# Performance work log

Hardware: AMD Instinct MI355X
Metric: run time of the kernel (lower is better)

Reference implementation:

```python
import jax, jax.numpy as jnp
import numpy as np

B, N, D, H, MLP = 8, 1024, 1024, 16, 4096
DEPTH = D // H
EPS = 1e-6
INV_SQRT_DEPTH = 1.0 / np.sqrt(DEPTH).astype(np.float32)


def _linear_params(key, fan_in, fan_out):
    w = jax.random.normal(key, (fan_in, fan_out), dtype=jnp.float32) * 0.02
    b = jnp.zeros((fan_out,), dtype=jnp.float32)
    return w, b


def setup_inputs() -> dict:
    key = jax.random.key(0)
    ks = jax.random.split(key, 20)
    inp = {}
    inp['inputs'] = jax.random.normal(ks[0], (B, N, D), dtype=jnp.float32)
    inp['z'] = jax.random.normal(ks[1], (B, D), dtype=jnp.float32)
    # norm1 conditioning MLPs
    inp['n1_hw'], inp['n1_hb'] = _linear_params(ks[2], D, D)
    inp['n1_gw'], inp['n1_gb'] = _linear_params(ks[3], D, D)
    inp['n1_bw'], inp['n1_bb'] = _linear_params(ks[4], D, D)
    # attention
    inp['wq_w'], inp['wq_b'] = _linear_params(ks[5], D, D)
    inp['wk_w'], inp['wk_b'] = _linear_params(ks[6], D, D)
    inp['wv_w'], inp['wv_b'] = _linear_params(ks[7], D, D)
    inp['qa_w'], inp['qa_b'] = _linear_params(ks[8], D, H)
    inp['out_w'], inp['out_b'] = _linear_params(ks[9], D, D)
    # norm2 conditioning MLPs
    inp['n2_hw'], inp['n2_hb'] = _linear_params(ks[10], D, D)
    inp['n2_gw'], inp['n2_gb'] = _linear_params(ks[11], D, D)
    inp['n2_bw'], inp['n2_bb'] = _linear_params(ks[12], D, D)
    # MLP
    inp['mlp_w1'], inp['mlp_b1'] = _linear_params(ks[13], D, MLP)
    inp['mlp_w2'], inp['mlp_b2'] = _linear_params(ks[14], MLP, D)
    return inp


def _sm_norm(x, z, hw, hb, gw, gb, bw, bb):
    # LayerNorm over last dim, no affine
    mean = jnp.mean(x, axis=-1, keepdims=True)
    var = jnp.mean(jnp.square(x - mean), axis=-1, keepdims=True)
    xn = (x - mean) / jnp.sqrt(var + EPS)
    h = jax.nn.relu(z @ hw + hb)                 # [B, D]
    scale = (h @ gw + gb)[:, :, None]            # [B, D, 1]
    shift = (h @ bw + bb)[:, :, None]            # [B, D, 1]
    # broadcasts since N == D (as in the torch module)
    return xn * scale + shift


def _additive_attn(x, wq_w, wq_b, wk_w, wk_b, wv_w, wv_b, qa_w, qa_b, out_w, out_b):
    q = x @ wq_w + wq_b                          # [B, N, D]
    k = x @ wk_w + wk_b
    v = x @ wv_w + wv_b
    attn = jnp.transpose(q @ qa_w + qa_b, (0, 2, 1)) * INV_SQRT_DEPTH  # [B, H, N]
    attn = jax.nn.softmax(attn, axis=-1)
    qh = q.reshape(B, N, H, DEPTH).transpose(0, 2, 1, 3)  # [B, H, N, d]
    kh = k.reshape(B, N, H, DEPTH).transpose(0, 2, 1, 3)
    vh = v.reshape(B, N, H, DEPTH).transpose(0, 2, 1, 3)
    global_q = jnp.einsum('bhn,bhnd->bhd', attn, qh)[:, :, None, :]  # [B, H, 1, d]
    r = global_q * kh * vh                       # [B, H, N, d]
    r = r.transpose(0, 2, 1, 3).reshape(B, N, D)
    return r @ out_w + out_b, attn


def reference(inputs, z,
              n1_hw, n1_hb, n1_gw, n1_gb, n1_bw, n1_bb,
              wq_w, wq_b, wk_w, wk_b, wv_w, wv_b, qa_w, qa_b, out_w, out_b,
              n2_hw, n2_hb, n2_gw, n2_gb, n2_bw, n2_bb,
              mlp_w1, mlp_b1, mlp_w2, mlp_b2):
    x_norm1 = _sm_norm(inputs, z, n1_hw, n1_hb, n1_gw, n1_gb, n1_bw, n1_bb)
    attn_out, attn_maps = _additive_attn(x_norm1, wq_w, wq_b, wk_w, wk_b,
                                         wv_w, wv_b, qa_w, qa_b, out_w, out_b)
    attn_out = inputs + attn_out                 # dropout rate 0 -> identity
    x_norm2 = _sm_norm(attn_out, z, n2_hw, n2_hb, n2_gw, n2_gb, n2_bw, n2_bb)
    h = jax.nn.gelu(x_norm2 @ mlp_w1 + mlp_b1, approximate=False)
    mlp_out = h @ mlp_w2 + mlp_b2
    output = attn_out + mlp_out
    return output, attn_maps
```

## Files before the change

kernel.cpp:

```cpp
#include <hip/hip_runtime.h>
#include <math.h>


typedef __attribute__((ext_vector_type(8))) short short8;
typedef __attribute__((ext_vector_type(4))) float f32x4;

#define DEVI __device__ __forceinline__

DEVI unsigned short f2bf(float f) {
  union { float f; unsigned int u; } c; c.f = f;
  unsigned int r = c.u + 0x7fffu + ((c.u >> 16) & 1u);
  return (unsigned short)(r >> 16);
}
DEVI float bf2f(unsigned short u) {
  union { unsigned int u; float f; } c; c.u = ((unsigned int)u) << 16;
  return c.f;
}

DEVI void async16(const void* g, void* l) {
  __builtin_amdgcn_global_load_lds((const __attribute__((address_space(1))) void*)g,
                                   (__attribute__((address_space(3))) void*)l, 16, 0, 0);
}

__global__ void transpose_bf16_k(const float* __restrict__ in,
                                 unsigned short* __restrict__ out, int R, int C) {
  __shared__ float tile[32][33];
  const int c0 = blockIdx.x * 32, r0 = blockIdx.y * 32;
  const int tx = threadIdx.x, ty = threadIdx.y;
#pragma unroll
  for (int j = 0; j < 4; j++) {
    int r = r0 + ty + j * 8, c = c0 + tx;
    if (r < R && c < C) tile[ty + j * 8][tx] = in[(size_t)r * C + c];
  }
  __syncthreads();
#pragma unroll
  for (int j = 0; j < 4; j++) {
    int c = c0 + ty + j * 8, r = r0 + tx;
    if (c < C && r < R) out[(size_t)c * R + r] = f2bf(tile[tx][ty + j * 8]);
  }
}

__global__ void pad_bias_k(const float* __restrict__ qa_b, float* __restrict__ pad) {
  int t = threadIdx.x;
  pad[t] = (t < 16) ? qa_b[t] : 0.f;
}

__global__ void zero_k(float4* __restrict__ p) {
  p[blockIdx.x * 256 + threadIdx.x] = float4{0.f, 0.f, 0.f, 0.f};
}

template <int NMAT>
__global__ __launch_bounds__(256) void skinny_k(const float* __restrict__ X,
                                                const float* __restrict__ W0,
                                                const float* __restrict__ W1,
                                                float* __restrict__ acc0,
                                                float* __restrict__ acc1) {
  const int tid = threadIdx.x;
  const int jt = blockIdx.x, kc = blockIdx.y;
  const int jl = tid & 63, kg = tid >> 6;
  const int jcol = jt * 64 + jl;
  __shared__ float xs[8][64];
  for (int i = tid; i < 512; i += 256) {
    const int b = i >> 6, kk = i & 63;
    xs[b][kk] = X[b * 1024 + kc * 64 + kk];
  }
  __syncthreads();
  float a0[8], a1[8];
#pragma unroll
  for (int b = 0; b < 8; b++) { a0[b] = 0.f; a1[b] = 0.f; }
#pragma unroll
  for (int kk = 0; kk < 16; kk++) {
    const int k = kg * 16 + kk;
    const float w0 = W0[(size_t)(kc * 64 + k) * 1024 + jcol];
#pragma unroll
    for (int b = 0; b < 8; b++) a0[b] += xs[b][k] * w0;
    if (NMAT == 2) {
      const float w1 = W1[(size_t)(kc * 64 + k) * 1024 + jcol];
#pragma unroll
      for (int b = 0; b < 8; b++) a1[b] += xs[b][k] * w1;
    }
  }
  __shared__ float red[256][9];
#pragma unroll
  for (int b = 0; b < 8; b++) red[tid][b] = a0[b];
  __syncthreads();
  if (tid < 64) {
#pragma unroll
    for (int b = 0; b < 8; b++) {
      const float s = red[tid][b] + red[tid + 64][b] + red[tid + 128][b] + red[tid + 192][b];
      atomicAdd(&acc0[b * 1024 + jcol], s);
    }
  }
  if (NMAT == 2) {
    __syncthreads();
#pragma unroll
    for (int b = 0; b < 8; b++) red[tid][b] = a1[b];
    __syncthreads();
    if (tid < 64) {
#pragma unroll
      for (int b = 0; b < 8; b++) {
        const float s = red[tid][b] + red[tid + 64][b] + red[tid + 128][b] + red[tid + 192][b];
        atomicAdd(&acc1[b * 1024 + jcol], s);
      }
    }
  }
}

__global__ void h_epi_k(const float* __restrict__ acc, const float* __restrict__ hb,
                        float* __restrict__ h) {
  const int i = blockIdx.x * 256 + threadIdx.x;
  h[i] = fmaxf(acc[i] + hb[i & 1023], 0.f);
}

__global__ __launch_bounds__(256) void ln_mod_k(const float* __restrict__ x,
                                                const float* __restrict__ s_acc,
                                                const float* __restrict__ t_acc,
                                                const float* __restrict__ gb,
                                                const float* __restrict__ bb,
                                                unsigned short* __restrict__ out) {
  const int lane = threadIdx.x & 63, wid = threadIdx.x >> 6;
  const size_t row = (size_t)blockIdx.x * 4 + wid;
  const int n = (int)(row & 1023);
  const float4* xr = (const float4*)(x + row * 1024);
  float4 v[4];
  float s = 0.f, ss = 0.f;
#pragma unroll
  for (int j = 0; j < 4; j++) {
    v[j] = xr[j * 64 + lane];
    s += v[j].x + v[j].y + v[j].z + v[j].w;
    ss += v[j].x * v[j].x + v[j].y * v[j].y + v[j].z * v[j].z + v[j].w * v[j].w;
  }
#pragma unroll
  for (int o = 32; o > 0; o >>= 1) { s += __shfl_xor(s, o); ss += __shfl_xor(ss, o); }
  const float mean = s * (1.f / 1024.f);
  const float var = ss * (1.f / 1024.f) - mean * mean;
  const float inv = rsqrtf(var + 1e-6f);
  const float scale = s_acc[row] + gb[n];
  const float shift = t_acc[row] + bb[n];
  const float sc = scale * inv;
  const float sh = shift - mean * sc;
#pragma unroll
  for (int j = 0; j < 4; j++) {
    ushort4 o4;
    o4.x = f2bf(v[j].x * sc + sh);
    o4.y = f2bf(v[j].y * sc + sh);
    o4.z = f2bf(v[j].z * sc + sh);
    o4.w = f2bf(v[j].w * sc + sh);
    *(ushort4*)(out + row * 1024 + (size_t)(j * 64 + lane) * 4) = o4;
  }
}

template <int EPI>
__global__ __launch_bounds__(256) void gemm_bf16(const unsigned short* __restrict__ A,
                                                 const unsigned short* __restrict__ BT,
                                                 const float* __restrict__ bias,
                                                 const float* __restrict__ resid,
                                                 void* __restrict__ Cout,
                                                 int M, int N, int K) {
  __shared__ unsigned short As[128 * 64];
  __shared__ unsigned short Bs[128 * 64];
  const int tid = threadIdx.x;
  const int lane = tid & 63, wid = tid >> 6;
  const int wr = wid >> 1, wc = wid & 1;
  const size_t brow = (size_t)blockIdx.y * 128;
  const size_t bcol = (size_t)blockIdx.x * 128;
  const unsigned short* Ab = A + brow * (size_t)K;
  const unsigned short* Bb = BT + bcol * (size_t)K;

  const f32x4 zero = {0.f, 0.f, 0.f, 0.f};
  f32x4 acc[4][4];
#pragma unroll
  for (int m = 0; m < 4; m++)
#pragma unroll
    for (int n = 0; n < 4; n++) acc[m][n] = zero;

  for (int k0 = 0; k0 < K; k0 += 64) {
#pragma unroll
    for (int i = 0; i < 4; i++) {
      const int eo = (i * 256 + tid) * 8;
      const int r = eo >> 6, c = eo & 63;
      async16(Ab + (size_t)r * K + (k0 + c), &As[eo]);
      async16(Bb + (size_t)r * K + (k0 + c), &Bs[eo]);
    }
    __syncthreads();
    const int lr = lane & 15, lk = (lane >> 4) * 8;
#pragma unroll
    for (int kk = 0; kk < 64; kk += 32) {
      short8 af[4], bfv[4];
#pragma unroll
      for (int m = 0; m < 4; m++)
        af[m] = *(const short8*)&As[(wr * 64 + m * 16 + lr) * 64 + kk + lk];
#pragma unroll
      for (int n = 0; n < 4; n++)
        bfv[n] = *(const short8*)&Bs[(wc * 64 + n * 16 + lr) * 64 + kk + lk];
#pragma unroll
      for (int m = 0; m < 4; m++)
#pragma unroll
        for (int n = 0; n < 4; n++)
          acc[m][n] = __builtin_amdgcn_mfma_f32_16x16x32_bf16(af[m], bfv[n], acc[m][n], 0, 0, 0);
    }
    __syncthreads();
  }

  const int lc = lane & 15, lr4 = (lane >> 4) * 4;
#pragma unroll
  for (int n = 0; n < 4; n++) {
    const size_t col = bcol + wc * 64 + n * 16 + lc;
    const float bv = bias[col];
#pragma unroll
    for (int m = 0; m < 4; m++) {
#pragma unroll
      for (int j = 0; j < 4; j++) {
        const size_t row = brow + wr * 64 + m * 16 + lr4 + j;
        const size_t idx = row * (size_t)N + col;
        float v = acc[m][n][j] + bv;
        if (EPI == 0) {
          ((unsigned short*)Cout)[idx] = f2bf(v);
        } else if (EPI == 1) {
          v = 0.5f * v * (1.0f + erff(v * 0.70710678118654752f));
          ((unsigned short*)Cout)[idx] = f2bf(v);
        } else if (EPI == 2) {
          ((float*)Cout)[idx] = v + resid[idx];
        } else {
          ((float*)Cout)[idx] = v;
        }
      }
    }
  }
}

__global__ __launch_bounds__(256) void softmax_k(const float* __restrict__ logits,
                                                 float* __restrict__ attn) {
  const int tid = threadIdx.x;
  const int bh = blockIdx.x;
  const int b = bh >> 4, h = bh & 15;
  __shared__ float redm[4];
  __shared__ float reds[4];
  float vals[4];
#pragma unroll
  for (int j = 0; j < 4; j++) {
    const int n = j * 256 + tid;
    vals[j] = logits[((size_t)b * 1024 + n) * 128 + h] * 0.125f;
  }
  float m = fmaxf(fmaxf(vals[0], vals[1]), fmaxf(vals[2], vals[3]));
#pragma unroll
  for (int o = 32; o > 0; o >>= 1) m = fmaxf(m, __shfl_xor(m, o));
  if ((tid & 63) == 0) redm[tid >> 6] = m;
  __syncthreads();
  m = fmaxf(fmaxf(redm[0], redm[1]), fmaxf(redm[2], redm[3]));
  float e[4];
  float s = 0.f;
#pragma unroll
  for (int j = 0; j < 4; j++) { e[j] = expf(vals[j] - m); s += e[j]; }
#pragma unroll
  for (int o = 32; o > 0; o >>= 1) s += __shfl_xor(s, o);
  if ((tid & 63) == 0) reds[tid >> 6] = s;
  __syncthreads();
  s = reds[0] + reds[1] + reds[2] + reds[3];
  const float invs = 1.f / s;
#pragma unroll
  for (int j = 0; j < 4; j++)
    attn[(size_t)bh * 1024 + j * 256 + tid] = e[j] * invs;
}

__global__ __launch_bounds__(256) void global_q_k(const float* __restrict__ attn,
                                                  const unsigned short* __restrict__ Q,
                                                  float* __restrict__ gq) {
  const int tid = threadIdx.x;
  const int bh = blockIdx.x;
  const int b = bh >> 4, h = bh & 15;
  const int d = tid & 63, g = tid >> 6;
  const float* arow = attn + (size_t)bh * 1024;
  const unsigned short* qcol = Q + (size_t)b * 1024 * 1024 + h * 64 + d;
  float acc = 0.f;
  for (int n = g * 256; n < g * 256 + 256; n++)
    acc += arow[n] * bf2f(qcol[(size_t)n * 1024]);
  __shared__ float red[256];
  red[tid] = acc;
  __syncthreads();
  if (g == 0) gq[(size_t)bh * 64 + d] = red[d] + red[64 + d] + red[128 + d] + red[192 + d];
}

__global__ __launch_bounds__(256) void r_k(const unsigned short* __restrict__ Kb,
                                           const unsigned short* __restrict__ Vb,
                                           const float* __restrict__ gq,
                                           unsigned short* __restrict__ R) {
  const size_t i = ((size_t)blockIdx.x * 256 + threadIdx.x) * 8;
  const int col = (int)(i & 1023);
  const size_t b = i >> 20;
  const int h = col >> 6, dd = col & 63;
  const float* g = gq + ((b << 4) + h) * 64 + dd;
  short8 kv = *(const short8*)(Kb + i);
  short8 vv = *(const short8*)(Vb + i);
  short8 r;
#pragma unroll
  for (int j = 0; j < 8; j++) {
    float f = g[j] * bf2f((unsigned short)kv[j]) * bf2f((unsigned short)vv[j]);
    r[j] = (short)f2bf(f);
  }
  *(short8*)(R + i) = r;
}

extern "C" void kernel_launch(void* const* d_in, const int* in_sizes, int n_in,
                              void* d_out, int out_size, void* d_ws, size_t ws_size,
                              hipStream_t stream) {
  (void)in_sizes; (void)n_in; (void)out_size; (void)ws_size;
  const float* inputs = (const float*)d_in[0];
  const float* z      = (const float*)d_in[1];
  const float* n1_hw = (const float*)d_in[2];  const float* n1_hb = (const float*)d_in[3];
  const float* n1_gw = (const float*)d_in[4];  const float* n1_gb = (const float*)d_in[5];
  const float* n1_bw = (const float*)d_in[6];  const float* n1_bb = (const float*)d_in[7];
  const float* wq_w  = (const float*)d_in[8];  const float* wq_b  = (const float*)d_in[9];
  const float* wk_w  = (const float*)d_in[10]; const float* wk_b  = (const float*)d_in[11];
  const float* wv_w  = (const float*)d_in[12]; const float* wv_b  = (const float*)d_in[13];
  const float* qa_w  = (const float*)d_in[14]; const float* qa_b  = (const float*)d_in[15];
  const float* out_w = (const float*)d_in[16]; const float* out_b = (const float*)d_in[17];
  const float* n2_hw = (const float*)d_in[18]; const float* n2_hb = (const float*)d_in[19];
  const float* n2_gw = (const float*)d_in[20]; const float* n2_gb = (const float*)d_in[21];
  const float* n2_bw = (const float*)d_in[22]; const float* n2_bb = (const float*)d_in[23];
  const float* mlp_w1 = (const float*)d_in[24]; const float* mlp_b1 = (const float*)d_in[25];
  const float* mlp_w2 = (const float*)d_in[26]; const float* mlp_b2 = (const float*)d_in[27];

  const int M = 8192, D = 1024, MLPD = 4096;

  char* ws = (char*)d_ws;
  size_t o = 0;
  auto alloc = [&](size_t bytes) -> char* {
    char* p = ws + o;
    o += (bytes + 255) & ~(size_t)255;
    return p;
  };
  unsigned short* wqT = (unsigned short*)alloc((size_t)D * D * 2);
  unsigned short* wkT = (unsigned short*)alloc((size_t)D * D * 2);
  unsigned short* wvT = (unsigned short*)alloc((size_t)D * D * 2);
  unsigned short* woT = (unsigned short*)alloc((size_t)D * D * 2);
  unsigned short* w1T = (unsigned short*)alloc((size_t)MLPD * D * 2);
  unsigned short* w2T = (unsigned short*)alloc((size_t)D * MLPD * 2);
  unsigned short* qaT = (unsigned short*)alloc((size_t)128 * D * 2);
  unsigned short* xn  = (unsigned short*)alloc((size_t)M * D * 2);
  char* big = alloc((size_t)M * MLPD * 2);
  unsigned short* Qb = (unsigned short*)big;
  unsigned short* Kb = (unsigned short*)(big + (size_t)M * D * 2);
  unsigned short* Vb = (unsigned short*)(big + (size_t)M * D * 4);
  float* logits      = (float*)(big + (size_t)M * D * 6);
  unsigned short* hbuf = (unsigned short*)big;
  float* cacc  = (float*)alloc(6 * 8192 * 4);
  float* accH1 = cacc;
  float* accS1 = cacc + 1 * 8192;
  float* accT1 = cacc + 2 * 8192;
  float* accH2 = cacc + 3 * 8192;
  float* accS2 = cacc + 4 * 8192;
  float* accT2 = cacc + 5 * 8192;
  float* h1     = (float*)alloc(8 * 1024 * 4);
  float* h2     = (float*)alloc(8 * 1024 * 4);
  float* gq     = (float*)alloc(8 * 16 * 64 * 4);
  float* qa_b_pad = (float*)alloc(128 * 4);

  float* out0 = (float*)d_out;
  float* attn = (float*)d_out + (size_t)M * D;

  const dim3 tb(32, 8);
  hipLaunchKernelGGL(transpose_bf16_k, dim3(32, 32), tb, 0, stream, wq_w, wqT, D, D);
  hipLaunchKernelGGL(transpose_bf16_k, dim3(32, 32), tb, 0, stream, wk_w, wkT, D, D);
  hipLaunchKernelGGL(transpose_bf16_k, dim3(32, 32), tb, 0, stream, wv_w, wvT, D, D);
  hipLaunchKernelGGL(transpose_bf16_k, dim3(32, 32), tb, 0, stream, out_w, woT, D, D);
  hipLaunchKernelGGL(transpose_bf16_k, dim3(128, 32), tb, 0, stream, mlp_w1, w1T, D, MLPD);
  hipLaunchKernelGGL(transpose_bf16_k, dim3(32, 128), tb, 0, stream, mlp_w2, w2T, MLPD, D);
  hipLaunchKernelGGL(transpose_bf16_k, dim3(1, 32), tb, 0, stream, qa_w, qaT, D, 16);
  hipLaunchKernelGGL(pad_bias_k, dim3(1), dim3(128), 0, stream, qa_b, qa_b_pad);

  hipLaunchKernelGGL(zero_k, dim3(48), dim3(256), 0, stream, (float4*)cacc);
  hipLaunchKernelGGL(skinny_k<1>, dim3(16, 16), dim3(256), 0, stream, z, n1_hw, (const float*)nullptr, accH1, (float*)nullptr);
  hipLaunchKernelGGL(h_epi_k, dim3(32), dim3(256), 0, stream, accH1, n1_hb, h1);
  hipLaunchKernelGGL(skinny_k<2>, dim3(16, 16), dim3(256), 0, stream, h1, n1_gw, n1_bw, accS1, accT1);
  hipLaunchKernelGGL(skinny_k<1>, dim3(16, 16), dim3(256), 0, stream, z, n2_hw, (const float*)nullptr, accH2, (float*)nullptr);
  hipLaunchKernelGGL(h_epi_k, dim3(32), dim3(256), 0, stream, accH2, n2_hb, h2);
  hipLaunchKernelGGL(skinny_k<2>, dim3(16, 16), dim3(256), 0, stream, h2, n2_gw, n2_bw, accS2, accT2);

  hipLaunchKernelGGL(ln_mod_k, dim3(M / 4), dim3(256), 0, stream, inputs, accS1, accT1, n1_gb, n1_bb, xn);

  hipLaunchKernelGGL(gemm_bf16<0>, dim3(8, 64), dim3(256), 0, stream, xn, wqT, wq_b, (const float*)nullptr, (void*)Qb, M, D, D);
  hipLaunchKernelGGL(gemm_bf16<0>, dim3(8, 64), dim3(256), 0, stream, xn, wkT, wk_b, (const float*)nullptr, (void*)Kb, M, D, D);
  hipLaunchKernelGGL(gemm_bf16<0>, dim3(8, 64), dim3(256), 0, stream, xn, wvT, wv_b, (const float*)nullptr, (void*)Vb, M, D, D);

  hipLaunchKernelGGL(gemm_bf16<3>, dim3(1, 64), dim3(256), 0, stream, Qb, qaT, qa_b_pad, (const float*)nullptr, (void*)logits, M, 128, D);

  hipLaunchKernelGGL(softmax_k, dim3(128), dim3(256), 0, stream, logits, attn);

  hipLaunchKernelGGL(global_q_k, dim3(128), dim3(256), 0, stream, attn, Qb, gq);

  hipLaunchKernelGGL(r_k, dim3(M * D / 8 / 256), dim3(256), 0, stream, Kb, Vb, gq, Kb);

  hipLaunchKernelGGL(gemm_bf16<2>, dim3(8, 64), dim3(256), 0, stream, Kb, woT, out_b, inputs, (void*)out0, M, D, D);

  hipLaunchKernelGGL(ln_mod_k, dim3(M / 4), dim3(256), 0, stream, out0, accS2, accT2, n2_gb, n2_bb, xn);

  hipLaunchKernelGGL(gemm_bf16<1>, dim3(32, 64), dim3(256), 0, stream, xn, w1T, mlp_b1, (const float*)nullptr, (void*)hbuf, M, MLPD, D);

  hipLaunchKernelGGL(gemm_bf16<2>, dim3(8, 64), dim3(256), 0, stream, hbuf, w2T, mlp_b2, out0, (void*)out0, M, D, MLPD);
}
```

Measured before the change: 682.4 us.

## Add double-buffered 256-wide GEMM kernel and fuse QKV projections into one launch

Adds a 512-thread GEMM with 256-column (and 128/256-row) tiles, double-buffered async global-to-LDS loads, XOR swizzled LDS layout and MFMA priority hints. All large GEMMs now use it. The Q, K and V projections are merged into one GEMM over a concatenated transposed weight and bias, with the epilogue scattering columns into the separate Q/K/V buffers. The intent is more data reuse per tile, load latency hidden behind compute, and fewer launches, at the cost of higher register and LDS use per block.

```diff
diff --git a/kernel.cpp b/kernel.cpp
--- a/kernel.cpp
+++ b/kernel.cpp
@@ -43,6 +43,12 @@
 __global__ void pad_bias_k(const float* __restrict__ qa_b, float* __restrict__ pad) {
   int t = threadIdx.x;
   pad[t] = (t < 16) ? qa_b[t] : 0.f;
+}
+
+__global__ void bias3_k(const float* __restrict__ b0, const float* __restrict__ b1,
+                        const float* __restrict__ b2, float* __restrict__ out) {
+  const int t = blockIdx.x * 256 + threadIdx.x;
+  out[t] = (t < 1024) ? b0[t] : (t < 2048 ? b1[t - 1024] : b2[t - 2048]);
 }
 
 __global__ void zero_k(float4* __restrict__ p) {
@@ -147,6 +153,120 @@
     o4.z = f2bf(v[j].z * sc + sh);
     o4.w = f2bf(v[j].w * sc + sh);
     *(ushort4*)(out + row * 1024 + (size_t)(j * 64 + lane) * 4) = o4;
+  }
+}
+
+template <int EPI, int BM>
+__global__ __launch_bounds__(512, 2) void gemm256(const unsigned short* __restrict__ A,
+                                                  const unsigned short* __restrict__ BT,
+                                                  const float* __restrict__ bias,
+                                                  const float* __restrict__ resid,
+                                                  void* __restrict__ Cout,
+                                                  int M, int N, int K) {
+  constexpr int WROWS = BM / 2;
+  constexpr int MF = WROWS / 16;
+  constexpr int ALOADS = (BM * 8) / 512;
+  constexpr int NLOADS = ALOADS + 4;
+  __shared__ unsigned short As[2][BM * 64];
+  __shared__ unsigned short Bs[2][256 * 64];
+  const int tid = threadIdx.x;
+  const int lane = tid & 63, w = tid >> 6;
+  const int wm = w >> 2, wn = w & 3;
+  const int lr = lane & 15;
+  const int g0 = lane >> 4;
+  const size_t brow = (size_t)blockIdx.y * BM;
+  const size_t bcol = (size_t)blockIdx.x * 256;
+  const unsigned short* Ab = A + brow * (size_t)K;
+  const unsigned short* Bb = BT + bcol * (size_t)K;
+  const int NT = K >> 6;
+
+  const f32x4 zero = {0.f, 0.f, 0.f, 0.f};
+  f32x4 acc[MF][4];
+#pragma unroll
+  for (int m = 0; m < MF; m++)
+#pragma unroll
+    for (int n = 0; n < 4; n++) acc[m][n] = zero;
+
+  auto stage = [&](int k0, int d) {
+#pragma unroll
+    for (int i = 0; i < ALOADS; i++) {
+      const int c = i * 512 + tid;
+      const int r = c >> 3, g = c & 7;
+      const int gl = g ^ (r & 7);
+      async16(Ab + (size_t)r * K + (k0 + gl * 8), &As[d][c * 8]);
+    }
+#pragma unroll
+    for (int i = 0; i < 4; i++) {
+      const int c = i * 512 + tid;
+      const int r = c >> 3, g = c & 7;
+      const int gl = g ^ (r & 7);
+      async16(Bb + (size_t)r * K + (k0 + gl * 8), &Bs[d][c * 8]);
+    }
+  };
+
+  stage(0, 0);
+  stage(64, 1);
+  if constexpr (NLOADS == 8) asm volatile("s_waitcnt vmcnt(8)" ::: "memory");
+  else asm volatile("s_waitcnt vmcnt(6)" ::: "memory");
+  __builtin_amdgcn_s_barrier();
+
+  for (int t = 0; t < NT; ++t) {
+    const unsigned short* as = As[t & 1];
+    const unsigned short* bs = Bs[t & 1];
+#pragma unroll
+    for (int kk = 0; kk < 64; kk += 32) {
+      const int gk = (kk >> 3) + g0;
+      short8 bfrag[4];
+#pragma unroll
+      for (int nf = 0; nf < 4; nf++) {
+        const int r = wn * 64 + nf * 16 + lr;
+        bfrag[nf] = *(const short8*)&bs[r * 64 + ((gk ^ (r & 7)) << 3)];
+      }
+      __builtin_amdgcn_s_setprio(1);
+#pragma unroll
+      for (int mf = 0; mf < MF; mf++) {
+        const int r = wm * WROWS + mf * 16 + lr;
+        const short8 afrag = *(const short8*)&as[r * 64 + ((gk ^ (r & 7)) << 3)];
+#pragma unroll
+        for (int nf = 0; nf < 4; nf++)
+          acc[mf][nf] = __builtin_amdgcn_mfma_f32_16x16x32_bf16(afrag, bfrag[nf], acc[mf][nf], 0, 0, 0);
+      }
+      __builtin_amdgcn_s_setprio(0);
+    }
+    asm volatile("" ::: "memory");
+    __builtin_amdgcn_s_barrier();
+    if (t + 2 < NT) {
+      stage((t + 2) << 6, t & 1);
+      if constexpr (NLOADS == 8) asm volatile("s_waitcnt vmcnt(8)" ::: "memory");
+      else asm volatile("s_waitcnt vmcnt(6)" ::: "memory");
+    } else {
+      asm volatile("s_waitcnt vmcnt(0)" ::: "memory");
+    }
+    __builtin_amdgcn_s_barrier();
+  }
+
+  const int lc = lane & 15, lrow = (lane >> 4) * 4;
+#pragma unroll
+  for (int nf = 0; nf < 4; nf++) {
+    const size_t col = bcol + wn * 64 + nf * 16 + lc;
+    const float bv = bias[col];
+#pragma unroll
+    for (int mf = 0; mf < MF; mf++) {
+#pragma unroll
+      for (int j = 0; j < 4; j++) {
+        const size_t row = brow + wm * WROWS + mf * 16 + lrow + j;
+        float v = acc[mf][nf][j] + bv;
+        if (EPI == 0) {
+          ((unsigned short*)Cout)[(size_t)(col >> 10) * ((size_t)M << 10) + row * 1024 + (col & 1023)] = f2bf(v);
+        } else if (EPI == 1) {
+          v = 0.5f * v * (1.0f + erff(v * 0.70710678118654752f));
+          ((unsigned short*)Cout)[row * (size_t)N + col] = f2bf(v);
+        } else {
+          const size_t idx = row * (size_t)N + col;
+          ((float*)Cout)[idx] = v + resid[idx];
+        }
+      }
+    }
   }
 }
 
@@ -213,17 +333,7 @@
       for (int j = 0; j < 4; j++) {
         const size_t row = brow + wr * 64 + m * 16 + lr4 + j;
         const size_t idx = row * (size_t)N + col;
-        float v = acc[m][n][j] + bv;
-        if (EPI == 0) {
-          ((unsigned short*)Cout)[idx] = f2bf(v);
-        } else if (EPI == 1) {
-          v = 0.5f * v * (1.0f + erff(v * 0.70710678118654752f));
-          ((unsigned short*)Cout)[idx] = f2bf(v);
-        } else if (EPI == 2) {
-          ((float*)Cout)[idx] = v + resid[idx];
-        } else {
-          ((float*)Cout)[idx] = v;
-        }
+        ((float*)Cout)[idx] = acc[m][n][j] + bv;
       }
     }
   }
@@ -330,9 +440,7 @@
     o += (bytes + 255) & ~(size_t)255;
     return p;
   };
-  unsigned short* wqT = (unsigned short*)alloc((size_t)D * D * 2);
-  unsigned short* wkT = (unsigned short*)alloc((size_t)D * D * 2);
-  unsigned short* wvT = (unsigned short*)alloc((size_t)D * D * 2);
+  unsigned short* wqkvT = (unsigned short*)alloc((size_t)3 * D * D * 2);
   unsigned short* woT = (unsigned short*)alloc((size_t)D * D * 2);
   unsigned short* w1T = (unsigned short*)alloc((size_t)MLPD * D * 2);
   unsigned short* w2T = (unsigned short*)alloc((size_t)D * MLPD * 2);
@@ -355,19 +463,21 @@
   float* h2     = (float*)alloc(8 * 1024 * 4);
   float* gq     = (float*)alloc(8 * 16 * 64 * 4);
   float* qa_b_pad = (float*)alloc(128 * 4);
+  float* qkvb    = (float*)alloc(3072 * 4);
 
   float* out0 = (float*)d_out;
   float* attn = (float*)d_out + (size_t)M * D;
 
   const dim3 tb(32, 8);
-  hipLaunchKernelGGL(transpose_bf16_k, dim3(32, 32), tb, 0, stream, wq_w, wqT, D, D);
-  hipLaunchKernelGGL(transpose_bf16_k, dim3(32, 32), tb, 0, stream, wk_w, wkT, D, D);
-  hipLaunchKernelGGL(transpose_bf16_k, dim3(32, 32), tb, 0, stream, wv_w, wvT, D, D);
+  hipLaunchKernelGGL(transpose_bf16_k, dim3(32, 32), tb, 0, stream, wq_w, wqkvT, D, D);
+  hipLaunchKernelGGL(transpose_bf16_k, dim3(32, 32), tb, 0, stream, wk_w, wqkvT + (size_t)D * D, D, D);
+  hipLaunchKernelGGL(transpose_bf16_k, dim3(32, 32), tb, 0, stream, wv_w, wqkvT + (size_t)2 * D * D, D, D);
   hipLaunchKernelGGL(transpose_bf16_k, dim3(32, 32), tb, 0, stream, out_w, woT, D, D);
   hipLaunchKernelGGL(transpose_bf16_k, dim3(128, 32), tb, 0, stream, mlp_w1, w1T, D, MLPD);
   hipLaunchKernelGGL(transpose_bf16_k, dim3(32, 128), tb, 0, stream, mlp_w2, w2T, MLPD, D);
   hipLaunchKernelGGL(transpose_bf16_k, dim3(1, 32), tb, 0, stream, qa_w, qaT, D, 16);
   hipLaunchKernelGGL(pad_bias_k, dim3(1), dim3(128), 0, stream, qa_b, qa_b_pad);
+  hipLaunchKernelGGL(bias3_k, dim3(12), dim3(256), 0, stream, wq_b, wk_b, wv_b, qkvb);
 
   hipLaunchKernelGGL(zero_k, dim3(48), dim3(256), 0, stream, (float4*)cacc);
   hipLaunchKernelGGL(skinny_k<1>, dim3(16, 16), dim3(256), 0, stream, z, n1_hw, (const float*)nullptr, accH1, (float*)nullptr);
@@ -379,9 +489,7 @@
 
   hipLaunchKernelGGL(ln_mod_k, dim3(M / 4), dim3(256), 0, stream, inputs, accS1, accT1, n1_gb, n1_bb, xn);
 
-  hipLaunchKernelGGL(gemm_bf16<0>, dim3(8, 64), dim3(256), 0, stream, xn, wqT, wq_b, (const float*)nullptr, (void*)Qb, M, D, D);
-  hipLaunchKernelGGL(gemm_bf16<0>, dim3(8, 64), dim3(256), 0, stream, xn, wkT, wk_b, (const float*)nullptr, (void*)Kb, M, D, D);
-  hipLaunchKernelGGL(gemm_bf16<0>, dim3(8, 64), dim3(256), 0, stream, xn, wvT, wv_b, (const float*)nullptr, (void*)Vb, M, D, D);
+  hipLaunchKernelGGL((gemm256<0, 256>), dim3(12, 32), dim3(512), 0, stream, xn, wqkvT, qkvb, (const float*)nullptr, (void*)Qb, M, 3072, D);
 
   hipLaunchKernelGGL(gemm_bf16<3>, dim3(1, 64), dim3(256), 0, stream, Qb, qaT, qa_b_pad, (const float*)nullptr, (void*)logits, M, 128, D);
 
@@ -391,11 +499,11 @@
 
   hipLaunchKernelGGL(r_k, dim3(M * D / 8 / 256), dim3(256), 0, stream, Kb, Vb, gq, Kb);
 
-  hipLaunchKernelGGL(gemm_bf16<2>, dim3(8, 64), dim3(256), 0, stream, Kb, woT, out_b, inputs, (void*)out0, M, D, D);
+  hipLaunchKernelGGL((gemm256<2, 128>), dim3(4, 64), dim3(512), 0, stream, Kb, woT, out_b, inputs, (void*)out0, M, D, D);
 
   hipLaunchKernelGGL(ln_mod_k, dim3(M / 4), dim3(256), 0, stream, out0, accS2, accT2, n2_gb, n2_bb, xn);
 
-  hipLaunchKernelGGL(gemm_bf16<1>, dim3(32, 64), dim3(256), 0, stream, xn, w1T, mlp_b1, (const float*)nullptr, (void*)hbuf, M, MLPD, D);
-
-  hipLaunchKernelGGL(gemm_bf16<2>, dim3(8, 64), dim3(256), 0, stream, hbuf, w2T, mlp_b2, out0, (void*)out0, M, D, MLPD);
-}
+  hipLaunchKernelGGL((gemm256<1, 256>), dim3(16, 32), dim3(512), 0, stream, xn, w1T, mlp_b1, (const float*)nullptr, (void*)hbuf, M, MLPD, D);
+
+  hipLaunchKernelGGL((gemm256<2, 128>), dim3(4, 64), dim3(512), 0, stream, hbuf, w2T, mlp_b2, out0, (void*)out0, M, D, MLPD);
+}
```

Measured after the change: 704.7 us. 1.03x slower.
